# Kernel optimization log

Hardware: AMD Instinct MI355X
Metric: run time of the kernel (lower is better)

The kernel has to match this reference:

```python
import jax, jax.numpy as jnp
import numpy as np

B, T = 128, 512
D_IN, D_OUT, H = 12, 320, 64


def _conv1d(x, w, b, dilation):
    # x: [B,C,T], w: [O,I,K]  (torch Conv1d layout), 'same' padding for odd receptive field
    k = w.shape[-1]
    pad = ((k - 1) * dilation + 1) // 2
    y = jax.lax.conv_general_dilated(x, w, (1,), [(pad, pad)], rhs_dilation=(dilation,),
                                     dimension_numbers=('NCH', 'OIH', 'NCH'))
    return y + b[None, :, None]


def _gelu(x):
    return jax.nn.gelu(x, approximate=False)  # torch F.gelu default (erf)


def _encoder(x, c0_1_w, c0_1_b, c0_2_w, c0_2_b, c1_p_w, c1_p_b, c1_1_w, c1_1_b, c1_2_w, c1_2_b):
    # TS2Vec DilatedConvEncoder, channels=[64, 320], kernel=3. x: [B,T,64] -> [B,T,320]
    h = x.transpose(0, 2, 1)  # [B,64,T]
    # block 0: 64->64, dilation 1, identity residual
    res = h
    t = _conv1d(_gelu(h), c0_1_w, c0_1_b, 1)
    t = _conv1d(_gelu(t), c0_2_w, c0_2_b, 1)
    h = t + res
    # block 1: 64->320, dilation 2, final -> 1x1 projector residual
    res = _conv1d(h, c1_p_w, c1_p_b, 1)
    t = _conv1d(_gelu(h), c1_1_w, c1_1_b, 2)
    t = _conv1d(_gelu(t), c1_2_w, c1_2_b, 2)
    h = t + res
    return h.transpose(0, 2, 1)  # [B,T,320]


def _gru_cell(x, h, wih, whh, bih, bhh):
    # torch.nn.GRUCell math
    gi = x @ wih.T + bih  # [B,3H]
    gh = h @ whh.T + bhh
    i_r, i_z, i_n = jnp.split(gi, 3, axis=-1)
    h_r, h_z, h_n = jnp.split(gh, 3, axis=-1)
    r = jax.nn.sigmoid(i_r + h_r)
    z = jax.nn.sigmoid(i_z + h_z)
    n = jnp.tanh(i_n + r * h_n)
    return (1.0 - z) * n + z * h


def setup_inputs() -> dict:
    key = jax.random.key(0)
    ks = iter(jax.random.split(key, 40))
    f = lambda shape, s=0.05: (jax.random.normal(next(ks), shape, dtype=jnp.float32) * s)
    inp = {
        'x1': jax.random.normal(next(ks), (B, T, D_IN), dtype=jnp.float32),
        'x2': jax.random.normal(next(ks), (B, T, D_IN), dtype=jnp.float32),
        'X1': jax.random.normal(next(ks), (B, T, D_IN), dtype=jnp.float32),
        'X2': jax.random.normal(next(ks), (B, T, D_IN), dtype=jnp.float32),
        'X': jax.random.normal(next(ks), (B, T, D_IN), dtype=jnp.float32),
        'w_in': f((D_IN, H)), 'b_in': f((H,)),
        'c0_1_w': f((H, H, 3)), 'c0_1_b': f((H,)),
        'c0_2_w': f((H, H, 3)), 'c0_2_b': f((H,)),
        'c1_p_w': f((D_OUT, H, 1)), 'c1_p_b': f((D_OUT,)),
        'c1_1_w': f((D_OUT, H, 3)), 'c1_1_b': f((D_OUT,)),
        'c1_2_w': f((D_OUT, D_OUT, 3)), 'c1_2_b': f((D_OUT,)),
        'ih_dense_w': f((D_OUT, 4 * D_OUT)), 'ih_dense_b': f((4 * D_OUT,)),
        'ih_proj_w': f((4 * D_OUT, D_IN)), 'ih_proj_b': f((D_IN,)),
        'fc_w': f((D_IN, D_OUT)), 'fc_b': f((D_OUT,)),
        'gru_wih': f((3 * H, D_OUT)), 'gru_whh': f((3 * H, H)),
        'gru_bih': f((3 * H,)), 'gru_bhh': f((3 * H,)),
        'out_w': f((H, D_OUT)), 'out_b': f((D_OUT,)),
        'fcr_w': f((D_OUT, D_IN)), 'fcr_b': f((D_IN,)),
    }
    return inp


def reference(x1, x2, X1, X2, X, w_in, b_in, c0_1_w, c0_1_b, c0_2_w, c0_2_b,
              c1_p_w, c1_p_b, c1_1_w, c1_1_b, c1_2_w, c1_2_b,
              ih_dense_w, ih_dense_b, ih_proj_w, ih_proj_b,
              fc_w, fc_b, gru_wih, gru_whh, gru_bih, gru_bhh,
              out_w, out_b, fcr_w, fcr_b):
    conv_p = (c0_1_w, c0_1_b, c0_2_w, c0_2_b, c1_p_w, c1_p_b, c1_1_w, c1_1_b, c1_2_w, c1_2_b)
    m1 = (x1 != 0).astype(jnp.int32)
    m2 = (x2 != 0).astype(jnp.int32)
    enc = lambda a: _encoder(a @ w_in + b_in, *conv_p)  # dropout = identity (deterministic ref)
    x_whole1 = enc(X1)
    x_whole2 = enc(X2)

    def interp(a):
        r = enc(a)
        h = jax.nn.relu(r @ ih_dense_w + ih_dense_b)
        return h @ ih_proj_w + ih_proj_b  # [B,T,D_IN]

    x_interp1 = interp(x1)
    x_interp2 = interp(x2)
    mask1 = (~jnp.isnan(x_interp1).any(-1)).astype(jnp.float32)  # [B,T]

    y1 = x_interp1 @ fc_w + fc_b  # [B,T,320] (self.fc applied to every step at once)
    y2 = x_interp2 @ fc_w + fc_b
    h0 = jnp.zeros((x1.shape[0], gru_whh.shape[1]), x1.dtype)

    def step(carry, xs):
        h1, h2 = carry
        yt1, yt2, mt = xs
        h1 = _gru_cell(yt1, h1, gru_wih, gru_whh, gru_bih, gru_bhh)
        h2 = _gru_cell(yt2, h2, gru_wih, gru_whh, gru_bih, gru_bhh)
        o1 = h1 @ out_w + out_b
        o2 = h2 @ out_w + out_b
        keep = (mt == 1.0)[:, None]
        o1 = jnp.where(keep, yt1, o1)
        o2 = jnp.where(keep, yt1, o2)  # faithful: source uses mask1 / y_t1 for both
        return (h1, h2), (o1, o2)

    _, (o1, o2) = jax.lax.scan(step, (h0, h0),
                               (y1.transpose(1, 0, 2), y2.transpose(1, 0, 2), mask1.T))
    outputs2 = jax.lax.stop_gradient(o2.transpose(1, 0, 2)) @ fcr_w + fcr_b
    outputs1 = jax.lax.stop_gradient(o1.transpose(1, 0, 2)) @ fcr_w + fcr_b
    return (x_whole1, x_whole2, outputs1, outputs2, m1, m2, x1, x2)
```

## Files before the change

### kernel.cpp

```cpp
#include <hip/hip_runtime.h>
#include <hip/hip_bf16.h>
#include <math.h>


#define BB    128
#define TSEQ  512
#define NTILE 8
#define DIN   12
#define C0    64
#define C1    320
#define TT    64
#define PP    76
#define HALO  6
#define R64P  72
#define R320P 328

#define S1 ((size_t)BB * TSEQ * C1)
#define S2 ((size_t)BB * TSEQ * DIN)

typedef __attribute__((ext_vector_type(8))) __bf16 bf16x8;
typedef __attribute__((ext_vector_type(4))) float f32x4;
#define MFMA16(a, b, c) __builtin_amdgcn_mfma_f32_16x16x32_bf16(a, b, c, 0, 0, 0)

#define O01 0
#define O02 12288
#define O11 24576
#define O12 86016
#define OD  413696
#define OP  823296
#define NWS 843776
#define OGM 843776
#define OF2 844064

#define LA  0
#define LB  10944
#define LC  10944
#define LXI 55552
#define LGM 58624
#define LF2 59200
#define LSZ 59248
#define LRR 0
#define LZB 41984

__device__ __forceinline__ float bf2f(const __hip_bfloat16 v) { return __bfloat162float(v); }
__device__ __forceinline__ __hip_bfloat16 f2bf(float f)       { return __float2bfloat16(f); }
__device__ __forceinline__ float geluf(float x) {
    return 0.5f * x * (1.0f + erff(x * 0.7071067811865475f));
}
__device__ __forceinline__ bf16x8 ldb8(const void* p) { return *(const bf16x8*)p; }

extern "C" __global__ void __launch_bounds__(256) prep_w(
    const float* __restrict__ c01w, const float* __restrict__ c02w,
    const float* __restrict__ c11w, const float* __restrict__ c12w,
    const float* __restrict__ c1pw, const float* __restrict__ dw,
    const float* __restrict__ pw,
    const float* __restrict__ fcw,  const float* __restrict__ fcb,
    const float* __restrict__ fcrw, const float* __restrict__ fcrb,
    __hip_bfloat16* __restrict__ ws)
{
    for (size_t i = (size_t)blockIdx.x * 256 + threadIdx.x; i < NWS;
         i += (size_t)gridDim.x * 256) {
        float v;
        if (i < O02)      { int q = (int)i;        int n = q / 192, r = q % 192;
                            v = c01w[(n * 64 + (r & 63)) * 3 + (r >> 6)]; }
        else if (i < O11) { int q = (int)(i - O02); int n = q / 192, r = q % 192;
                            v = c02w[(n * 64 + (r & 63)) * 3 + (r >> 6)]; }
        else if (i < O12) { int q = (int)(i - O11); int n = q / 192, r = q % 192;
                            v = c11w[(n * 64 + (r & 63)) * 3 + (r >> 6)]; }
        else if (i < OD)  { int q = (int)(i - O12); int n = q >> 10, k = q & 1023;
                            v = (k < 960) ? c12w[(n * 320 + (k % 320)) * 3 + (k / 320)]
                                          : c1pw[n * 64 + (k - 960)]; }
        else if (i < OP)  { int q = (int)(i - OD);  int h = q / 320, c = q % 320;
                            v = dw[c * 1280 + h]; }
        else              { int q = (int)(i - OP);  int j = q / 1280, h = q % 1280;
                            v = (j < 12) ? pw[h * 12 + j] : 0.f; }
        ws[i] = f2bf(v);
    }
    if (blockIdx.x == 0) {
        float* gm = (float*)(ws + OGM);
        float* f2 = (float*)(ws + OF2);
        for (int o = threadIdx.x; o < 144; o += 256) {
            int j = o / 12, j2 = o - j * 12;
            float s = 0.f;
            for (int c = 0; c < C1; c++) s += fcw[j * C1 + c] * fcrw[c * 12 + j2];
            gm[o] = s;
        }
        if (threadIdx.x < 12) {
            float s = fcrb[threadIdx.x];
            for (int c = 0; c < C1; c++) s += fcb[c] * fcrw[c * 12 + threadIdx.x];
            f2[threadIdx.x] = s;
        }
    }
}

extern "C" __global__ void __launch_bounds__(256, 2) fused_main(
    const float* __restrict__ x1,  const float* __restrict__ X1,
    const float* __restrict__ X2,
    const float* __restrict__ w_in, const float* __restrict__ b_in,
    const float* __restrict__ c01b, const float* __restrict__ c02b,
    const float* __restrict__ c1pb, const float* __restrict__ c11b,
    const float* __restrict__ c12b,
    const float* __restrict__ db,   const float* __restrict__ pb,
    const __hip_bfloat16* __restrict__ ws,
    float* __restrict__ out)
{
    __shared__ __align__(16) unsigned char smem[LSZ];
    __hip_bfloat16* A  = (__hip_bfloat16*)(smem + LA);
    __hip_bfloat16* Bf = (__hip_bfloat16*)(smem + LB);
    __hip_bfloat16* C  = (__hip_bfloat16*)(smem + LC);
    float* XI = (float*)(smem + LXI);
    float* Gm = (float*)(smem + LGM);
    float* F2 = (float*)(smem + LF2);
    __hip_bfloat16* Rr = (__hip_bfloat16*)(smem + LRR);

    const int tid  = threadIdx.x;
    const int wv   = tid >> 6;
    const int lane = tid & 63;
    const int lm   = lane & 15;
    const int lq   = lane >> 4;
    const int bid  = blockIdx.x;
    const int pass = bid % 3;
    const int rem  = bid / 3;
    const int b    = rem >> 3;
    const int t0   = (rem & (NTILE - 1)) * TT;
    const float* xin = (pass == 0) ? X1 : (pass == 1) ? X2 : x1;

    const f32x4 Z4 = {0.f, 0.f, 0.f, 0.f};

    if (pass == 2) {
        const float* gmw = (const float*)(ws + OGM);
        const float* f2w = (const float*)(ws + OF2);
        for (int o = tid; o < 144; o += 256) Gm[o] = gmw[o];
        if (tid < 12) F2[tid] = f2w[tid];
        for (int o = tid; o < TT * 12; o += 256) XI[o] = pb[o % 12];
    }

    for (int o = tid; o < PP * C0; o += 256) {
        int p = o >> 6, c = o & 63;
        int t = t0 + p - HALO;
        float acc = 0.f;
        if (t >= 0 && t < TSEQ) {
            acc = b_in[c];
            const float4* xr4 = (const float4*)(xin + ((size_t)b * TSEQ + t) * DIN);
            float4 v0 = xr4[0], v1 = xr4[1], v2 = xr4[2];
            const float xv[12] = {v0.x, v0.y, v0.z, v0.w, v1.x, v1.y,
                                  v1.z, v1.w, v2.x, v2.y, v2.z, v2.w};
            #pragma unroll
            for (int i = 0; i < DIN; i++) acc += xv[i] * w_in[i * C0 + c];
        }
        A [p * R64P + c] = f2bf(acc);
        Bf[p * R64P + c] = f2bf(geluf(acc));
    }
    __syncthreads();

    {
        const int oc = wv * 16 + lm;
        f32x4 acc[5] = {Z4, Z4, Z4, Z4, Z4};
        #pragma unroll
        for (int ks = 0; ks < 6; ks++) {
            int tap = ks >> 1, ci = ((ks & 1) << 5) + (lq << 3);
            bf16x8 bf = ldb8(ws + O01 + oc * 192 + ks * 32 + (lq << 3));
            #pragma unroll
            for (int mt = 0; mt < 5; mt++) {
                int p = 1 + mt * 16 + lm + tap - 1; p = p > 75 ? 75 : p;
                acc[mt] = MFMA16(ldb8(Bf + p * R64P + ci), bf, acc[mt]);
            }
        }
        __syncthreads();
        float bias = c01b[oc];
        #pragma unroll
        for (int mt = 0; mt < 5; mt++)
            #pragma unroll
            for (int r = 0; r < 4; r++) {
                int m = mt * 16 + lq * 4 + r;
                if (m < 74) {
                    int p = 1 + m, t = t0 + p - HALO;
                    Bf[p * R64P + oc] =
                        f2bf((t >= 0 && t < TSEQ) ? geluf(acc[mt][r] + bias) : 0.f);
                }
            }
    }
    __syncthreads();

    {
        const int oc = wv * 16 + lm;
        f32x4 acc[5] = {Z4, Z4, Z4, Z4, Z4};
        #pragma unroll
        for (int ks = 0; ks < 6; ks++) {
            int tap = ks >> 1, ci = ((ks & 1) << 5) + (lq << 3);
            bf16x8 bf = ldb8(ws + O02 + oc * 192 + ks * 32 + (lq << 3));
            #pragma unroll
            for (int mt = 0; mt < 5; mt++) {
                int p = 2 + mt * 16 + lm + tap - 1; p = p > 75 ? 75 : p;
                acc[mt] = MFMA16(ldb8(Bf + p * R64P + ci), bf, acc[mt]);
            }
        }
        float resv[5][4];
        #pragma unroll
        for (int mt = 0; mt < 5; mt++)
            #pragma unroll
            for (int r = 0; r < 4; r++) {
                int m = mt * 16 + lq * 4 + r;
                resv[mt][r] = (m < 72) ? bf2f(A[(2 + m) * R64P + oc]) : 0.f;
            }
        __syncthreads();
        float bias = c02b[oc];
        #pragma unroll
        for (int mt = 0; mt < 5; mt++)
            #pragma unroll
            for (int r = 0; r < 4; r++) {
                int m = mt * 16 + lq * 4 + r;
                if (m < 72) {
                    int p = 2 + m, t = t0 + p - HALO;
                    bool v = (t >= 0 && t < TSEQ);
                    float hb = acc[mt][r] + bias + resv[mt][r];
                    A [p * R64P + oc] = f2bf(v ? hb : 0.f);
                    Bf[p * R64P + oc] = f2bf(v ? geluf(hb) : 0.f);
                }
            }
    }
    __syncthreads();

    {
        f32x4 acc[5][5];
        #pragma unroll
        for (int mt = 0; mt < 5; mt++)
            #pragma unroll
            for (int nt = 0; nt < 5; nt++) acc[mt][nt] = Z4;
        bf16x8 aa[5], ba[5], ab[5], bb[5];
        auto ld3 = [&](int ks, bf16x8 (&a)[5], bf16x8 (&bw)[5]) {
            int tap = ks >> 1, ci = ((ks & 1) << 5) + (lq << 3);
            #pragma unroll
            for (int mt = 0; mt < 5; mt++) {
                int p = 4 + mt * 16 + lm + 2 * (tap - 1); p = p > 75 ? 75 : p;
                a[mt] = ldb8(Bf + p * R64P + ci);
            }
            #pragma unroll
            for (int nt = 0; nt < 5; nt++)
                bw[nt] = ldb8(ws + O11 + (wv * 80 + nt * 16 + lm) * 192
                              + ks * 32 + (lq << 3));
        };
        ld3(0, aa, ba);
        #pragma unroll
        for (int ks = 0; ks < 6; ks += 2) {
            ld3(ks + 1, ab, bb);
            #pragma unroll
            for (int nt = 0; nt < 5; nt++)
                #pragma unroll
                for (int mt = 0; mt < 5; mt++)
                    acc[mt][nt] = MFMA16(aa[mt], ba[nt], acc[mt][nt]);
            if (ks + 2 < 6) ld3(ks + 2, aa, ba);
            #pragma unroll
            for (int nt = 0; nt < 5; nt++)
                #pragma unroll
                for (int mt = 0; mt < 5; mt++)
                    acc[mt][nt] = MFMA16(ab[mt], bb[nt], acc[mt][nt]);
        }
        __syncthreads();
        #pragma unroll
        for (int nt = 0; nt < 5; nt++) {
            int oc = wv * 80 + nt * 16 + lm;
            float bias = c11b[oc];
            #pragma unroll
            for (int mt = 0; mt < 5; mt++)
                #pragma unroll
                for (int r = 0; r < 4; r++) {
                    int m = mt * 16 + lq * 4 + r;
                    if (m < 68) {
                        int t = t0 + 4 + m - HALO;
                        C[m * R320P + oc] =
                            f2bf((t >= 0 && t < TSEQ) ? geluf(acc[mt][nt][r] + bias) : 0.f);
                    }
                }
        }
    }
    __syncthreads();

    {
        f32x4 acc[4][5];
        #pragma unroll
        for (int mt = 0; mt < 4; mt++)
            #pragma unroll
            for (int nt = 0; nt < 5; nt++) acc[mt][nt] = Z4;
        bf16x8 aa[4], ba[5], ab[4], bb[5];
        auto ld4 = [&](int ks, bf16x8 (&a)[4], bf16x8 (&bw)[5]) {
            if (ks < 30) {
                int tap = (ks >= 20) ? 2 : (ks >= 10 ? 1 : 0);
                int ci = (ks - tap * 10) * 32 + (lq << 3);
                #pragma unroll
                for (int mt = 0; mt < 4; mt++)
                    a[mt] = ldb8(C + (2 + mt * 16 + lm + 2 * (tap - 1)) * R320P + ci);
            } else {
                int ci = ((ks - 30) << 5) + (lq << 3);
                #pragma unroll
                for (int mt = 0; mt < 4; mt++)
                    a[mt] = ldb8(A + (6 + mt * 16 + lm) * R64P + ci);
            }
            #pragma unroll
            for (int nt = 0; nt < 5; nt++)
                bw[nt] = ldb8(ws + O12 + (wv * 80 + nt * 16 + lm) * 1024
                              + ks * 32 + (lq << 3));
        };
        ld4(0, aa, ba);
        for (int ks = 0; ks < 32; ks += 2) {
            ld4(ks + 1, ab, bb);
            #pragma unroll
            for (int nt = 0; nt < 5; nt++)
                #pragma unroll
                for (int mt = 0; mt < 4; mt++)
                    acc[mt][nt] = MFMA16(aa[mt], ba[nt], acc[mt][nt]);
            if (ks + 2 < 32) ld4(ks + 2, aa, ba);
            #pragma unroll
            for (int nt = 0; nt < 5; nt++)
                #pragma unroll
                for (int mt = 0; mt < 4; mt++)
                    acc[mt][nt] = MFMA16(ab[mt], bb[nt], acc[mt][nt]);
        }
        if (pass < 2) {
            #pragma unroll
            for (int nt = 0; nt < 5; nt++) {
                int oc = wv * 80 + nt * 16 + lm;
                float bias = c12b[oc] + c1pb[oc];
                const size_t obase = (pass == 1) ? S1 : (size_t)0;
                #pragma unroll
                for (int mt = 0; mt < 4; mt++)
                    #pragma unroll
                    for (int r = 0; r < 4; r++) {
                        int m = mt * 16 + lq * 4 + r;
                        out[obase + ((size_t)b * TSEQ + t0 + m) * C1 + oc] =
                            acc[mt][nt][r] + bias;
                    }
            }
        } else {
            __syncthreads();
            #pragma unroll
            for (int nt = 0; nt < 5; nt++) {
                int oc = wv * 80 + nt * 16 + lm;
                float bias = c12b[oc] + c1pb[oc];
                #pragma unroll
                for (int mt = 0; mt < 4; mt++)
                    #pragma unroll
                    for (int r = 0; r < 4; r++) {
                        int m = mt * 16 + lq * 4 + r;
                        Rr[m * R320P + oc] = f2bf(acc[mt][nt][r] + bias);
                    }
            }
            __syncthreads();
        }
    }

    if (pass == 2) {
        __hip_bfloat16* zb = (__hip_bfloat16*)(smem + LZB) + wv * (16 * R64P);
        f32x4 xacc[4] = {Z4, Z4, Z4, Z4};
        for (int cn = 0; cn < 5; cn++) {
            const int h0 = wv * 320 + cn * 64;
            f32x4 dacc[4][4];
            #pragma unroll
            for (int mt = 0; mt < 4; mt++)
                #pragma unroll
                for (int nt = 0; nt < 4; nt++) dacc[mt][nt] = Z4;
            bf16x8 aa[4], ba[4], ab[4], bb[4];
            auto ldd = [&](int ks, bf16x8 (&a)[4], bf16x8 (&bw)[4]) {
                int ci = ks * 32 + (lq << 3);
                #pragma unroll
                for (int mt = 0; mt < 4; mt++)
                    a[mt] = ldb8(Rr + (mt * 16 + lm) * R320P + ci);
                #pragma unroll
                for (int nt = 0; nt < 4; nt++)
                    bw[nt] = ldb8(ws + OD + (h0 + nt * 16 + lm) * 320 + ci);
            };
            ldd(0, aa, ba);
            #pragma unroll
            for (int ks = 0; ks < 10; ks += 2) {
                ldd(ks + 1, ab, bb);
                #pragma unroll
                for (int nt = 0; nt < 4; nt++)
                    #pragma unroll
                    for (int mt = 0; mt < 4; mt++)
                        dacc[mt][nt] = MFMA16(aa[mt], ba[nt], dacc[mt][nt]);
                if (ks + 2 < 10) ldd(ks + 2, aa, ba);
                #pragma unroll
                for (int nt = 0; nt < 4; nt++)
                    #pragma unroll
                    for (int mt = 0; mt < 4; mt++)
                        dacc[mt][nt] = MFMA16(ab[mt], bb[nt], dacc[mt][nt]);
            }
            #pragma unroll
            for (int mt = 0; mt < 4; mt++) {
                #pragma unroll
                for (int nt = 0; nt < 4; nt++) {
                    int h = h0 + nt * 16 + lm;
                    float dbv = db[h];
                    #pragma unroll
                    for (int r = 0; r < 4; r++)
                        zb[(lq * 4 + r) * R64P + nt * 16 + lm] =
                            f2bf(fmaxf(dacc[mt][nt][r] + dbv, 0.f));
                }
                #pragma unroll
                for (int k2 = 0; k2 < 2; k2++) {
                    int hl = k2 * 32 + (lq << 3);
                    bf16x8 bf = ldb8(ws + OP + lm * 1280 + h0 + hl);
                    xacc[mt] = MFMA16(ldb8(zb + lm * R64P + hl), bf, xacc[mt]);
                }
            }
        }
        if (lm < 12) {
            #pragma unroll
            for (int mt = 0; mt < 4; mt++)
                #pragma unroll
                for (int r = 0; r < 4; r++)
                    atomicAdd(&XI[(mt * 16 + lq * 4 + r) * 12 + lm], xacc[mt][r]);
        }
        __syncthreads();
        for (int o = tid; o < TT * 12; o += 256) {
            int p = o / 12, j2 = o - p * 12;
            float val = F2[j2];
            #pragma unroll
            for (int j = 0; j < 12; j++) val += XI[p * 12 + j] * Gm[j * 12 + j2];
            size_t idx = ((size_t)b * TSEQ + t0 + p) * DIN + j2;
            out[2 * S1 + idx]      = val;
            out[2 * S1 + S2 + idx] = val;
        }
    }
}

extern "C" __global__ void __launch_bounds__(256) tail_kernel(
    const float* __restrict__ x1, const float* __restrict__ x2,
    float* __restrict__ out)
{
    size_t i = (size_t)blockIdx.x * 256 + threadIdx.x;
    if (i >= S2) return;
    float a = x1[i], c = x2[i];
    const size_t base = 2 * S1 + 2 * S2;
    out[base + i]          = (a != 0.f) ? 1.f : 0.f;
    out[base + S2 + i]     = (c != 0.f) ? 1.f : 0.f;
    out[base + 2 * S2 + i] = a;
    out[base + 3 * S2 + i] = c;
}

extern "C" void kernel_launch(void* const* d_in, const int* in_sizes, int n_in,
                              void* d_out, int out_size, void* d_ws, size_t ws_size,
                              hipStream_t stream)
{
    (void)in_sizes; (void)n_in; (void)ws_size; (void)out_size;
    const float* x1   = (const float*)d_in[0];
    const float* x2   = (const float*)d_in[1];
    const float* X1   = (const float*)d_in[2];
    const float* X2   = (const float*)d_in[3];
    const float* w_in = (const float*)d_in[5];
    const float* b_in = (const float*)d_in[6];
    const float* c01w = (const float*)d_in[7];
    const float* c01b = (const float*)d_in[8];
    const float* c02w = (const float*)d_in[9];
    const float* c02b = (const float*)d_in[10];
    const float* c1pw = (const float*)d_in[11];
    const float* c1pb = (const float*)d_in[12];
    const float* c11w = (const float*)d_in[13];
    const float* c11b = (const float*)d_in[14];
    const float* c12w = (const float*)d_in[15];
    const float* c12b = (const float*)d_in[16];
    const float* dwp  = (const float*)d_in[17];
    const float* dbp  = (const float*)d_in[18];
    const float* pwp  = (const float*)d_in[19];
    const float* pbp  = (const float*)d_in[20];
    const float* fcw  = (const float*)d_in[21];
    const float* fcb  = (const float*)d_in[22];
    const float* fcrw = (const float*)d_in[29];
    const float* fcrb = (const float*)d_in[30];
    float* out = (float*)d_out;
    __hip_bfloat16* ws = (__hip_bfloat16*)d_ws;

    prep_w<<<824, 256, 0, stream>>>(c01w, c02w, c11w, c12w, c1pw, dwp, pwp,
                                    fcw, fcb, fcrw, fcrb, ws);

    fused_main<<<3 * BB * NTILE, 256, 0, stream>>>(
        x1, X1, X2, w_in, b_in, c01b, c02b, c1pb, c11b, c12b,
        dbp, pbp, ws, out);

    tail_kernel<<<(int)((S2 + 255) / 256), 256, 0, stream>>>(x1, x2, out);
}
```

Baseline: 826.0 us.

## Double workgroup to 512 threads and split M tiles across two wave groups

Each block now runs 8 waves instead of 4. Waves are split into four output-channel groups times two M-row groups, so each wave holds half as many accumulators across all conv, GEMM and decoder stages. Conv weights for the small layers are preloaded into registers, and the LDS layout grows to give each of the 8 waves its own zb scratch area. The aim is lower register pressure and more waves to hide latency. In exchange, each weight fragment is loaded from global memory by both M groups, and the 5-tile stages leave one group with uneven work.

```diff
diff --git a/kernel.cpp b/kernel.cpp
--- a/kernel.cpp
+++ b/kernel.cpp
@@ -35,10 +35,10 @@
 #define LA  0
 #define LB  10944
 #define LC  10944
-#define LXI 55552
-#define LGM 58624
-#define LF2 59200
-#define LSZ 59248
+#define LXI 60416
+#define LGM 63488
+#define LF2 64064
+#define LSZ 64112
 #define LRR 0
 #define LZB 41984
 
@@ -93,7 +93,7 @@
     }
 }
 
-extern "C" __global__ void __launch_bounds__(256, 2) fused_main(
+extern "C" __global__ void __launch_bounds__(512, 4) fused_main(
     const float* __restrict__ x1,  const float* __restrict__ X1,
     const float* __restrict__ X2,
     const float* __restrict__ w_in, const float* __restrict__ b_in,
@@ -115,6 +115,8 @@
 
     const int tid  = threadIdx.x;
     const int wv   = tid >> 6;
+    const int wg   = wv & 3;
+    const int mg   = wv >> 2;
     const int lane = tid & 63;
     const int lm   = lane & 15;
     const int lq   = lane >> 4;
@@ -130,12 +132,12 @@
     if (pass == 2) {
         const float* gmw = (const float*)(ws + OGM);
         const float* f2w = (const float*)(ws + OF2);
-        for (int o = tid; o < 144; o += 256) Gm[o] = gmw[o];
+        for (int o = tid; o < 144; o += 512) Gm[o] = gmw[o];
         if (tid < 12) F2[tid] = f2w[tid];
-        for (int o = tid; o < TT * 12; o += 256) XI[o] = pb[o % 12];
-    }
-
-    for (int o = tid; o < PP * C0; o += 256) {
+        for (int o = tid; o < TT * 12; o += 512) XI[o] = pb[o % 12];
+    }
+
+    for (int o = tid; o < PP * C0; o += 512) {
         int p = o >> 6, c = o & 63;
         int t = t0 + p - HALO;
         float acc = 0.f;
@@ -154,122 +156,87 @@
     __syncthreads();
 
     {
-        const int oc = wv * 16 + lm;
-        f32x4 acc[5] = {Z4, Z4, Z4, Z4, Z4};
+        const int oc = wg * 16 + lm;
+        bf16x8 bw[6];
+        #pragma unroll
+        for (int ks = 0; ks < 6; ks++)
+            bw[ks] = ldb8(ws + O01 + oc * 192 + ks * 32 + (lq << 3));
+        f32x4 acc[3] = {Z4, Z4, Z4};
         #pragma unroll
         for (int ks = 0; ks < 6; ks++) {
             int tap = ks >> 1, ci = ((ks & 1) << 5) + (lq << 3);
-            bf16x8 bf = ldb8(ws + O01 + oc * 192 + ks * 32 + (lq << 3));
-            #pragma unroll
-            for (int mt = 0; mt < 5; mt++) {
-                int p = 1 + mt * 16 + lm + tap - 1; p = p > 75 ? 75 : p;
-                acc[mt] = MFMA16(ldb8(Bf + p * R64P + ci), bf, acc[mt]);
+            #pragma unroll
+            for (int kk = 0; kk < 3; kk++) {
+                int mt = mg + 2 * kk;
+                if (mt < 5) {
+                    int p = 1 + mt * 16 + lm + tap - 1; p = p > 75 ? 75 : p;
+                    acc[kk] = MFMA16(ldb8(Bf + p * R64P + ci), bw[ks], acc[kk]);
+                }
             }
         }
         __syncthreads();
         float bias = c01b[oc];
         #pragma unroll
-        for (int mt = 0; mt < 5; mt++)
+        for (int kk = 0; kk < 3; kk++) {
+            int mt = mg + 2 * kk;
+            if (mt < 5)
+                #pragma unroll
+                for (int r = 0; r < 4; r++) {
+                    int m = mt * 16 + lq * 4 + r;
+                    if (m < 74) {
+                        int p = 1 + m, t = t0 + p - HALO;
+                        Bf[p * R64P + oc] =
+                            f2bf((t >= 0 && t < TSEQ) ? geluf(acc[kk][r] + bias) : 0.f);
+                    }
+                }
+        }
+    }
+    __syncthreads();
+
+    {
+        const int oc = wg * 16 + lm;
+        bf16x8 bw[6];
+        #pragma unroll
+        for (int ks = 0; ks < 6; ks++)
+            bw[ks] = ldb8(ws + O02 + oc * 192 + ks * 32 + (lq << 3));
+        f32x4 acc[3] = {Z4, Z4, Z4};
+        #pragma unroll
+        for (int ks = 0; ks < 6; ks++) {
+            int tap = ks >> 1, ci = ((ks & 1) << 5) + (lq << 3);
+            #pragma unroll
+            for (int kk = 0; kk < 3; kk++) {
+                int mt = mg + 2 * kk;
+                if (mt < 5) {
+                    int p = 2 + mt * 16 + lm + tap - 1; p = p > 75 ? 75 : p;
+                    acc[kk] = MFMA16(ldb8(Bf + p * R64P + ci), bw[ks], acc[kk]);
+                }
+            }
+        }
+        float resv[3][4];
+        #pragma unroll
+        for (int kk = 0; kk < 3; kk++) {
+            int mt = mg + 2 * kk;
             #pragma unroll
             for (int r = 0; r < 4; r++) {
                 int m = mt * 16 + lq * 4 + r;
-                if (m < 74) {
-                    int p = 1 + m, t = t0 + p - HALO;
-                    Bf[p * R64P + oc] =
-                        f2bf((t >= 0 && t < TSEQ) ? geluf(acc[mt][r] + bias) : 0.f);
-                }
-            }
-    }
-    __syncthreads();
-
-    {
-        const int oc = wv * 16 + lm;
-        f32x4 acc[5] = {Z4, Z4, Z4, Z4, Z4};
-        #pragma unroll
-        for (int ks = 0; ks < 6; ks++) {
-            int tap = ks >> 1, ci = ((ks & 1) << 5) + (lq << 3);
-            bf16x8 bf = ldb8(ws + O02 + oc * 192 + ks * 32 + (lq << 3));
-            #pragma unroll
-            for (int mt = 0; mt < 5; mt++) {
-                int p = 2 + mt * 16 + lm + tap - 1; p = p > 75 ? 75 : p;
-                acc[mt] = MFMA16(ldb8(Bf + p * R64P + ci), bf, acc[mt]);
-            }
-        }
-        float resv[5][4];
-        #pragma unroll
-        for (int mt = 0; mt < 5; mt++)
-            #pragma unroll
-            for (int r = 0; r < 4; r++) {
-                int m = mt * 16 + lq * 4 + r;
-                resv[mt][r] = (m < 72) ? bf2f(A[(2 + m) * R64P + oc]) : 0.f;
-            }
+                resv[kk][r] = (mt < 5 && m < 72) ? bf2f(A[(2 + m) * R64P + oc]) : 0.f;
+            }
+        }
         __syncthreads();
         float bias = c02b[oc];
         #pragma unroll
-        for (int mt = 0; mt < 5; mt++)
-            #pragma unroll
-            for (int r = 0; r < 4; r++) {
-                int m = mt * 16 + lq * 4 + r;
-                if (m < 72) {
-                    int p = 2 + m, t = t0 + p - HALO;
-                    bool v = (t >= 0 && t < TSEQ);
-                    float hb = acc[mt][r] + bias + resv[mt][r];
-                    A [p * R64P + oc] = f2bf(v ? hb : 0.f);
-                    Bf[p * R64P + oc] = f2bf(v ? geluf(hb) : 0.f);
-                }
-            }
-    }
-    __syncthreads();
-
-    {
-        f32x4 acc[5][5];
-        #pragma unroll
-        for (int mt = 0; mt < 5; mt++)
-            #pragma unroll
-            for (int nt = 0; nt < 5; nt++) acc[mt][nt] = Z4;
-        bf16x8 aa[5], ba[5], ab[5], bb[5];
-        auto ld3 = [&](int ks, bf16x8 (&a)[5], bf16x8 (&bw)[5]) {
-            int tap = ks >> 1, ci = ((ks & 1) << 5) + (lq << 3);
-            #pragma unroll
-            for (int mt = 0; mt < 5; mt++) {
-                int p = 4 + mt * 16 + lm + 2 * (tap - 1); p = p > 75 ? 75 : p;
-                a[mt] = ldb8(Bf + p * R64P + ci);
-            }
-            #pragma unroll
-            for (int nt = 0; nt < 5; nt++)
-                bw[nt] = ldb8(ws + O11 + (wv * 80 + nt * 16 + lm) * 192
-                              + ks * 32 + (lq << 3));
-        };
-        ld3(0, aa, ba);
-        #pragma unroll
-        for (int ks = 0; ks < 6; ks += 2) {
-            ld3(ks + 1, ab, bb);
-            #pragma unroll
-            for (int nt = 0; nt < 5; nt++)
-                #pragma unroll
-                for (int mt = 0; mt < 5; mt++)
-                    acc[mt][nt] = MFMA16(aa[mt], ba[nt], acc[mt][nt]);
-            if (ks + 2 < 6) ld3(ks + 2, aa, ba);
-            #pragma unroll
-            for (int nt = 0; nt < 5; nt++)
-                #pragma unroll
-                for (int mt = 0; mt < 5; mt++)
-                    acc[mt][nt] = MFMA16(ab[mt], bb[nt], acc[mt][nt]);
-        }
-        __syncthreads();
-        #pragma unroll
-        for (int nt = 0; nt < 5; nt++) {
-            int oc = wv * 80 + nt * 16 + lm;
-            float bias = c11b[oc];
-            #pragma unroll
-            for (int mt = 0; mt < 5; mt++)
+        for (int kk = 0; kk < 3; kk++) {
+            int mt = mg + 2 * kk;
+            if (mt < 5)
                 #pragma unroll
                 for (int r = 0; r < 4; r++) {
                     int m = mt * 16 + lq * 4 + r;
-                    if (m < 68) {
-                        int t = t0 + 4 + m - HALO;
-                        C[m * R320P + oc] =
-                            f2bf((t >= 0 && t < TSEQ) ? geluf(acc[mt][nt][r] + bias) : 0.f);
+                    if (m < 72) {
+                        int p = 2 + m, t = t0 + p - HALO;
+                        bool v = (t >= 0 && t < TSEQ);
+                        float hb = acc[kk][r] + bias + resv[kk][r];
+                        A [p * R64P + oc] = f2bf(v ? hb : 0.f);
+                        Bf[p * R64P + oc] = f2bf(v ? geluf(hb) : 0.f);
                     }
                 }
         }
@@ -277,28 +244,91 @@
     __syncthreads();
 
     {
-        f32x4 acc[4][5];
-        #pragma unroll
-        for (int mt = 0; mt < 4; mt++)
-            #pragma unroll
-            for (int nt = 0; nt < 5; nt++) acc[mt][nt] = Z4;
-        bf16x8 aa[4], ba[5], ab[4], bb[5];
-        auto ld4 = [&](int ks, bf16x8 (&a)[4], bf16x8 (&bw)[5]) {
+        f32x4 acc[3][5];
+        #pragma unroll
+        for (int kk = 0; kk < 3; kk++)
+            #pragma unroll
+            for (int nt = 0; nt < 5; nt++) acc[kk][nt] = Z4;
+        bf16x8 bcur[5], bnxt[5];
+        #pragma unroll
+        for (int nt = 0; nt < 5; nt++)
+            bcur[nt] = ldb8(ws + O11 + (wg * 80 + nt * 16 + lm) * 192 + (lq << 3));
+        #pragma unroll
+        for (int ks = 0; ks < 6; ks++) {
+            if (ks < 5)
+                #pragma unroll
+                for (int nt = 0; nt < 5; nt++)
+                    bnxt[nt] = ldb8(ws + O11 + (wg * 80 + nt * 16 + lm) * 192
+                                    + (ks + 1) * 32 + (lq << 3));
+            int tap = ks >> 1, ci = ((ks & 1) << 5) + (lq << 3);
+            bf16x8 a[3];
+            #pragma unroll
+            for (int kk = 0; kk < 3; kk++) {
+                int mt = mg + 2 * kk;
+                if (mt < 5) {
+                    int p = 4 + mt * 16 + lm + 2 * (tap - 1); p = p > 75 ? 75 : p;
+                    a[kk] = ldb8(Bf + p * R64P + ci);
+                }
+            }
+            #pragma unroll
+            for (int nt = 0; nt < 5; nt++)
+                #pragma unroll
+                for (int kk = 0; kk < 3; kk++)
+                    if (mg + 2 * kk < 5)
+                        acc[kk][nt] = MFMA16(a[kk], bcur[nt], acc[kk][nt]);
+            #pragma unroll
+            for (int nt = 0; nt < 5; nt++) bcur[nt] = bnxt[nt];
+        }
+        __syncthreads();
+        #pragma unroll
+        for (int nt = 0; nt < 5; nt++) {
+            int oc = wg * 80 + nt * 16 + lm;
+            float bias = c11b[oc];
+            #pragma unroll
+            for (int kk = 0; kk < 3; kk++) {
+                int mt = mg + 2 * kk;
+                if (mt < 5)
+                    #pragma unroll
+                    for (int r = 0; r < 4; r++) {
+                        int m = mt * 16 + lq * 4 + r;
+                        if (m < 68) {
+                            int t = t0 + 4 + m - HALO;
+                            C[m * R320P + oc] =
+                                f2bf((t >= 0 && t < TSEQ) ? geluf(acc[kk][nt][r] + bias) : 0.f);
+                        }
+                    }
+            }
+        }
+    }
+    __syncthreads();
+
+    {
+        f32x4 acc[2][5];
+        #pragma unroll
+        for (int kk = 0; kk < 2; kk++)
+            #pragma unroll
+            for (int nt = 0; nt < 5; nt++) acc[kk][nt] = Z4;
+        bf16x8 aa[2], ba[5], ab[2], bb[5];
+        auto ld4 = [&](int ks, bf16x8 (&a)[2], bf16x8 (&bw)[5]) {
             if (ks < 30) {
                 int tap = (ks >= 20) ? 2 : (ks >= 10 ? 1 : 0);
                 int ci = (ks - tap * 10) * 32 + (lq << 3);
                 #pragma unroll
-                for (int mt = 0; mt < 4; mt++)
-                    a[mt] = ldb8(C + (2 + mt * 16 + lm + 2 * (tap - 1)) * R320P + ci);
+                for (int kk = 0; kk < 2; kk++) {
+                    int mt = mg + 2 * kk;
+                    a[kk] = ldb8(C + (2 + mt * 16 + lm + 2 * (tap - 1)) * R320P + ci);
+                }
             } else {
                 int ci = ((ks - 30) << 5) + (lq << 3);
                 #pragma unroll
-                for (int mt = 0; mt < 4; mt++)
-                    a[mt] = ldb8(A + (6 + mt * 16 + lm) * R64P + ci);
+                for (int kk = 0; kk < 2; kk++) {
+                    int mt = mg + 2 * kk;
+                    a[kk] = ldb8(A + (6 + mt * 16 + lm) * R64P + ci);
+                }
             }
             #pragma unroll
             for (int nt = 0; nt < 5; nt++)
-                bw[nt] = ldb8(ws + O12 + (wv * 80 + nt * 16 + lm) * 1024
+                bw[nt] = ldb8(ws + O12 + (wg * 80 + nt * 16 + lm) * 1024
                               + ks * 32 + (lq << 3));
         };
         ld4(0, aa, ba);
@@ -307,43 +337,47 @@
             #pragma unroll
             for (int nt = 0; nt < 5; nt++)
                 #pragma unroll
-                for (int mt = 0; mt < 4; mt++)
-                    acc[mt][nt] = MFMA16(aa[mt], ba[nt], acc[mt][nt]);
+                for (int kk = 0; kk < 2; kk++)
+                    acc[kk][nt] = MFMA16(aa[kk], ba[nt], acc[kk][nt]);
             if (ks + 2 < 32) ld4(ks + 2, aa, ba);
             #pragma unroll
             for (int nt = 0; nt < 5; nt++)
                 #pragma unroll
-                for (int mt = 0; mt < 4; mt++)
-                    acc[mt][nt] = MFMA16(ab[mt], bb[nt], acc[mt][nt]);
+                for (int kk = 0; kk < 2; kk++)
+                    acc[kk][nt] = MFMA16(ab[kk], bb[nt], acc[kk][nt]);
         }
         if (pass < 2) {
             #pragma unroll
             for (int nt = 0; nt < 5; nt++) {
-                int oc = wv * 80 + nt * 16 + lm;
+                int oc = wg * 80 + nt * 16 + lm;
                 float bias = c12b[oc] + c1pb[oc];
                 const size_t obase = (pass == 1) ? S1 : (size_t)0;
                 #pragma unroll
-                for (int mt = 0; mt < 4; mt++)
+                for (int kk = 0; kk < 2; kk++) {
+                    int mt = mg + 2 * kk;
                     #pragma unroll
                     for (int r = 0; r < 4; r++) {
                         int m = mt * 16 + lq * 4 + r;
                         out[obase + ((size_t)b * TSEQ + t0 + m) * C1 + oc] =
-                            acc[mt][nt][r] + bias;
+                            acc[kk][nt][r] + bias;
                     }
+                }
             }
         } else {
             __syncthreads();
             #pragma unroll
             for (int nt = 0; nt < 5; nt++) {
-                int oc = wv * 80 + nt * 16 + lm;
+                int oc = wg * 80 + nt * 16 + lm;
                 float bias = c12b[oc] + c1pb[oc];
                 #pragma unroll
-                for (int mt = 0; mt < 4; mt++)
+                for (int kk = 0; kk < 2; kk++) {
+                    int mt = mg + 2 * kk;
                     #pragma unroll
                     for (int r = 0; r < 4; r++) {
                         int m = mt * 16 + lq * 4 + r;
-                        Rr[m * R320P + oc] = f2bf(acc[mt][nt][r] + bias);
+                        Rr[m * R320P + oc] = f2bf(acc[kk][nt][r] + bias);
                     }
+                }
             }
             __syncthreads();
         }
@@ -351,20 +385,20 @@
 
     if (pass == 2) {
         __hip_bfloat16* zb = (__hip_bfloat16*)(smem + LZB) + wv * (16 * R64P);
-        f32x4 xacc[4] = {Z4, Z4, Z4, Z4};
+        f32x4 xacc[2] = {Z4, Z4};
         for (int cn = 0; cn < 5; cn++) {
-            const int h0 = wv * 320 + cn * 64;
-            f32x4 dacc[4][4];
-            #pragma unroll
-            for (int mt = 0; mt < 4; mt++)
-                #pragma unroll
-                for (int nt = 0; nt < 4; nt++) dacc[mt][nt] = Z4;
-            bf16x8 aa[4], ba[4], ab[4], bb[4];
-            auto ldd = [&](int ks, bf16x8 (&a)[4], bf16x8 (&bw)[4]) {
+            const int h0 = wg * 320 + cn * 64;
+            f32x4 dacc[2][4];
+            #pragma unroll
+            for (int kk = 0; kk < 2; kk++)
+                #pragma unroll
+                for (int nt = 0; nt < 4; nt++) dacc[kk][nt] = Z4;
+            bf16x8 aa[2], ba[4], ab[2], bb[4];
+            auto ldd = [&](int ks, bf16x8 (&a)[2], bf16x8 (&bw)[4]) {
                 int ci = ks * 32 + (lq << 3);
                 #pragma unroll
-                for (int mt = 0; mt < 4; mt++)
-                    a[mt] = ldb8(Rr + (mt * 16 + lm) * R320P + ci);
+                for (int kk = 0; kk < 2; kk++)
+                    a[kk] = ldb8(Rr + ((mg + 2 * kk) * 16 + lm) * R320P + ci);
                 #pragma unroll
                 for (int nt = 0; nt < 4; nt++)
                     bw[nt] = ldb8(ws + OD + (h0 + nt * 16 + lm) * 320 + ci);
@@ -376,17 +410,17 @@
                 #pragma unroll
                 for (int nt = 0; nt < 4; nt++)
                     #pragma unroll
-                    for (int mt = 0; mt < 4; mt++)
-                        dacc[mt][nt] = MFMA16(aa[mt], ba[nt], dacc[mt][nt]);
+                    for (int kk = 0; kk < 2; kk++)
+                        dacc[kk][nt] = MFMA16(aa[kk], ba[nt], dacc[kk][nt]);
                 if (ks + 2 < 10) ldd(ks + 2, aa, ba);
                 #pragma unroll
                 for (int nt = 0; nt < 4; nt++)
                     #pragma unroll
-                    for (int mt = 0; mt < 4; mt++)
-                        dacc[mt][nt] = MFMA16(ab[mt], bb[nt], dacc[mt][nt]);
-            }
-            #pragma unroll
-            for (int mt = 0; mt < 4; mt++) {
+                    for (int kk = 0; kk < 2; kk++)
+                        dacc[kk][nt] = MFMA16(ab[kk], bb[nt], dacc[kk][nt]);
+            }
+            #pragma unroll
+            for (int kk = 0; kk < 2; kk++) {
                 #pragma unroll
                 for (int nt = 0; nt < 4; nt++) {
                     int h = h0 + nt * 16 + lm;
@@ -394,25 +428,27 @@
                     #pragma unroll
                     for (int r = 0; r < 4; r++)
                         zb[(lq * 4 + r) * R64P + nt * 16 + lm] =
-                            f2bf(fmaxf(dacc[mt][nt][r] + dbv, 0.f));
+                            f2bf(fmaxf(dacc[kk][nt][r] + dbv, 0.f));
                 }
                 #pragma unroll
                 for (int k2 = 0; k2 < 2; k2++) {
                     int hl = k2 * 32 + (lq << 3);
                     bf16x8 bf = ldb8(ws + OP + lm * 1280 + h0 + hl);
-                    xacc[mt] = MFMA16(ldb8(zb + lm * R64P + hl), bf, xacc[mt]);
+                    xacc[kk] = MFMA16(ldb8(zb + lm * R64P + hl), bf, xacc[kk]);
                 }
             }
         }
         if (lm < 12) {
             #pragma unroll
-            for (int mt = 0; mt < 4; mt++)
+            for (int kk = 0; kk < 2; kk++) {
+                int mt = mg + 2 * kk;
                 #pragma unroll
                 for (int r = 0; r < 4; r++)
-                    atomicAdd(&XI[(mt * 16 + lq * 4 + r) * 12 + lm], xacc[mt][r]);
+                    atomicAdd(&XI[(mt * 16 + lq * 4 + r) * 12 + lm], xacc[kk][r]);
+            }
         }
         __syncthreads();
-        for (int o = tid; o < TT * 12; o += 256) {
+        for (int o = tid; o < TT * 12; o += 512) {
             int p = o / 12, j2 = o - p * 12;
             float val = F2[j2];
             #pragma unroll
@@ -473,7 +509,7 @@
     prep_w<<<824, 256, 0, stream>>>(c01w, c02w, c11w, c12w, c1pw, dwp, pwp,
                                     fcw, fcb, fcrw, fcrb, ws);
 
-    fused_main<<<3 * BB * NTILE, 256, 0, stream>>>(
+    fused_main<<<3 * BB * NTILE, 512, 0, stream>>>(
         x1, X1, X2, w_in, b_in, c01b, c02b, c1pb, c11b, c12b,
         dbp, pbp, ws, out);
 
```

Measured after the change: 1.262 ms. 1.53x slower.

## Swizzle 320-wide LDS tiles, shrink LDS, and raise occupancy to three blocks

Applied to the files above, without the earlier changes.

Replaces the padded 328-element row layout of the C and Rr LDS buffers with an unpadded 640-byte row plus an XOR swizzle, which reduces LDS footprint and avoids bank conflicts. The smem layout is repacked, and the pass-2 constant loads move later so they reuse freed space. Launch bounds go from 2 to 3 blocks per CU. Register-level double buffering of LDS A operands is dropped in favour of loading A just before use, with weight-operand prefetch kept. The goal is more concurrent waves to hide latency, at the cost of tighter register budgets and possible spills.

```diff
diff --git a/kernel.cpp b/kernel.cpp
--- a/kernel.cpp
+++ b/kernel.cpp
@@ -13,7 +13,6 @@
 #define PP    76
 #define HALO  6
 #define R64P  72
-#define R320P 328
 
 #define S1 ((size_t)BB * TSEQ * C1)
 #define S2 ((size_t)BB * TSEQ * DIN)
@@ -33,14 +32,14 @@
 #define OF2 844064
 
 #define LA  0
-#define LB  10944
-#define LC  10944
-#define LXI 55552
-#define LGM 58624
-#define LF2 59200
-#define LSZ 59248
+#define LB  10656
+#define LC  10656
+#define LSZ 54176
 #define LRR 0
-#define LZB 41984
+#define LZB 40960
+#define LXI 50176
+#define LGM 53248
+#define LF2 53824
 
 __device__ __forceinline__ float bf2f(const __hip_bfloat16 v) { return __bfloat162float(v); }
 __device__ __forceinline__ __hip_bfloat16 f2bf(float f)       { return __float2bfloat16(f); }
@@ -48,6 +47,9 @@
     return 0.5f * x * (1.0f + erff(x * 0.7071067811865475f));
 }
 __device__ __forceinline__ bf16x8 ldb8(const void* p) { return *(const bf16x8*)p; }
+__device__ __forceinline__ void* swp(void* base, int row, int col) {
+    return (void*)((unsigned char*)base + (((row * 640 + col * 2)) ^ ((row & 7) << 4)));
+}
 
 extern "C" __global__ void __launch_bounds__(256) prep_w(
     const float* __restrict__ c01w, const float* __restrict__ c02w,
@@ -93,7 +95,7 @@
     }
 }
 
-extern "C" __global__ void __launch_bounds__(256, 2) fused_main(
+extern "C" __global__ void __launch_bounds__(256, 3) fused_main(
     const float* __restrict__ x1,  const float* __restrict__ X1,
     const float* __restrict__ X2,
     const float* __restrict__ w_in, const float* __restrict__ b_in,
@@ -107,11 +109,11 @@
     __shared__ __align__(16) unsigned char smem[LSZ];
     __hip_bfloat16* A  = (__hip_bfloat16*)(smem + LA);
     __hip_bfloat16* Bf = (__hip_bfloat16*)(smem + LB);
-    __hip_bfloat16* C  = (__hip_bfloat16*)(smem + LC);
+    unsigned char*  Cb = smem + LC;
+    unsigned char*  Rb = smem + LRR;
     float* XI = (float*)(smem + LXI);
     float* Gm = (float*)(smem + LGM);
     float* F2 = (float*)(smem + LF2);
-    __hip_bfloat16* Rr = (__hip_bfloat16*)(smem + LRR);
 
     const int tid  = threadIdx.x;
     const int wv   = tid >> 6;
@@ -127,14 +129,6 @@
 
     const f32x4 Z4 = {0.f, 0.f, 0.f, 0.f};
 
-    if (pass == 2) {
-        const float* gmw = (const float*)(ws + OGM);
-        const float* f2w = (const float*)(ws + OF2);
-        for (int o = tid; o < 144; o += 256) Gm[o] = gmw[o];
-        if (tid < 12) F2[tid] = f2w[tid];
-        for (int o = tid; o < TT * 12; o += 256) XI[o] = pb[o % 12];
-    }
-
     for (int o = tid; o < PP * C0; o += 256) {
         int p = o >> 6, c = o & 63;
         int t = t0 + p - HALO;
@@ -148,22 +142,25 @@
             #pragma unroll
             for (int i = 0; i < DIN; i++) acc += xv[i] * w_in[i * C0 + c];
         }
-        A [p * R64P + c] = f2bf(acc);
+        if (p < 74) A[p * R64P + c] = f2bf(acc);
         Bf[p * R64P + c] = f2bf(geluf(acc));
     }
     __syncthreads();
 
     {
         const int oc = wv * 16 + lm;
+        bf16x8 bw[6];
+        #pragma unroll
+        for (int ks = 0; ks < 6; ks++)
+            bw[ks] = ldb8(ws + O01 + oc * 192 + ks * 32 + (lq << 3));
         f32x4 acc[5] = {Z4, Z4, Z4, Z4, Z4};
         #pragma unroll
         for (int ks = 0; ks < 6; ks++) {
             int tap = ks >> 1, ci = ((ks & 1) << 5) + (lq << 3);
-            bf16x8 bf = ldb8(ws + O01 + oc * 192 + ks * 32 + (lq << 3));
             #pragma unroll
             for (int mt = 0; mt < 5; mt++) {
                 int p = 1 + mt * 16 + lm + tap - 1; p = p > 75 ? 75 : p;
-                acc[mt] = MFMA16(ldb8(Bf + p * R64P + ci), bf, acc[mt]);
+                acc[mt] = MFMA16(ldb8(Bf + p * R64P + ci), bw[ks], acc[mt]);
             }
         }
         __syncthreads();
@@ -184,15 +181,18 @@
 
     {
         const int oc = wv * 16 + lm;
+        bf16x8 bw[6];
+        #pragma unroll
+        for (int ks = 0; ks < 6; ks++)
+            bw[ks] = ldb8(ws + O02 + oc * 192 + ks * 32 + (lq << 3));
         f32x4 acc[5] = {Z4, Z4, Z4, Z4, Z4};
         #pragma unroll
         for (int ks = 0; ks < 6; ks++) {
             int tap = ks >> 1, ci = ((ks & 1) << 5) + (lq << 3);
-            bf16x8 bf = ldb8(ws + O02 + oc * 192 + ks * 32 + (lq << 3));
             #pragma unroll
             for (int mt = 0; mt < 5; mt++) {
                 int p = 2 + mt * 16 + lm + tap - 1; p = p > 75 ? 75 : p;
-                acc[mt] = MFMA16(ldb8(Bf + p * R64P + ci), bf, acc[mt]);
+                acc[mt] = MFMA16(ldb8(Bf + p * R64P + ci), bw[ks], acc[mt]);
             }
         }
         float resv[5][4];
@@ -227,34 +227,23 @@
         for (int mt = 0; mt < 5; mt++)
             #pragma unroll
             for (int nt = 0; nt < 5; nt++) acc[mt][nt] = Z4;
-        bf16x8 aa[5], ba[5], ab[5], bb[5];
-        auto ld3 = [&](int ks, bf16x8 (&a)[5], bf16x8 (&bw)[5]) {
+        #pragma unroll
+        for (int ks = 0; ks < 6; ks++) {
             int tap = ks >> 1, ci = ((ks & 1) << 5) + (lq << 3);
+            bf16x8 a[5];
             #pragma unroll
             for (int mt = 0; mt < 5; mt++) {
                 int p = 4 + mt * 16 + lm + 2 * (tap - 1); p = p > 75 ? 75 : p;
                 a[mt] = ldb8(Bf + p * R64P + ci);
             }
             #pragma unroll
-            for (int nt = 0; nt < 5; nt++)
-                bw[nt] = ldb8(ws + O11 + (wv * 80 + nt * 16 + lm) * 192
-                              + ks * 32 + (lq << 3));
-        };
-        ld3(0, aa, ba);
-        #pragma unroll
-        for (int ks = 0; ks < 6; ks += 2) {
-            ld3(ks + 1, ab, bb);
-            #pragma unroll
-            for (int nt = 0; nt < 5; nt++)
+            for (int nt = 0; nt < 5; nt++) {
+                bf16x8 bw = ldb8(ws + O11 + (wv * 80 + nt * 16 + lm) * 192
+                                 + ks * 32 + (lq << 3));
                 #pragma unroll
                 for (int mt = 0; mt < 5; mt++)
-                    acc[mt][nt] = MFMA16(aa[mt], ba[nt], acc[mt][nt]);
-            if (ks + 2 < 6) ld3(ks + 2, aa, ba);
-            #pragma unroll
-            for (int nt = 0; nt < 5; nt++)
-                #pragma unroll
-                for (int mt = 0; mt < 5; mt++)
-                    acc[mt][nt] = MFMA16(ab[mt], bb[nt], acc[mt][nt]);
+                    acc[mt][nt] = MFMA16(a[mt], bw, acc[mt][nt]);
+            }
         }
         __syncthreads();
         #pragma unroll
@@ -268,7 +257,7 @@
                     int m = mt * 16 + lq * 4 + r;
                     if (m < 68) {
                         int t = t0 + 4 + m - HALO;
-                        C[m * R320P + oc] =
+                        *(__hip_bfloat16*)swp(Cb, m, oc) =
                             f2bf((t >= 0 && t < TSEQ) ? geluf(acc[mt][nt][r] + bias) : 0.f);
                     }
                 }
@@ -279,42 +268,64 @@
     {
         f32x4 acc[4][5];
         #pragma unroll
-        for (int mt = 0; mt < 4; mt++)
-            #pragma unroll
-            for (int nt = 0; nt < 5; nt++) acc[mt][nt] = Z4;
-        bf16x8 aa[4], ba[5], ab[4], bb[5];
-        auto ld4 = [&](int ks, bf16x8 (&a)[4], bf16x8 (&bw)[5]) {
-            if (ks < 30) {
-                int tap = (ks >= 20) ? 2 : (ks >= 10 ? 1 : 0);
-                int ci = (ks - tap * 10) * 32 + (lq << 3);
-                #pragma unroll
-                for (int mt = 0; mt < 4; mt++)
-                    a[mt] = ldb8(C + (2 + mt * 16 + lm + 2 * (tap - 1)) * R320P + ci);
-            } else {
-                int ci = ((ks - 30) << 5) + (lq << 3);
-                #pragma unroll
-                for (int mt = 0; mt < 4; mt++)
-                    a[mt] = ldb8(A + (6 + mt * 16 + lm) * R64P + ci);
-            }
+        for (int kk = 0; kk < 4; kk++)
+            #pragma unroll
+            for (int nt = 0; nt < 5; nt++) acc[kk][nt] = Z4;
+        bf16x8 ba[5], bb[5];
+        #pragma unroll
+        for (int nt = 0; nt < 5; nt++)
+            ba[nt] = ldb8(ws + O12 + (wv * 80 + nt * 16 + lm) * 1024 + (lq << 3));
+        for (int ks = 0; ks < 32; ks += 2) {
             #pragma unroll
             for (int nt = 0; nt < 5; nt++)
-                bw[nt] = ldb8(ws + O12 + (wv * 80 + nt * 16 + lm) * 1024
-                              + ks * 32 + (lq << 3));
-        };
-        ld4(0, aa, ba);
-        for (int ks = 0; ks < 32; ks += 2) {
-            ld4(ks + 1, ab, bb);
-            #pragma unroll
-            for (int nt = 0; nt < 5; nt++)
-                #pragma unroll
-                for (int mt = 0; mt < 4; mt++)
-                    acc[mt][nt] = MFMA16(aa[mt], ba[nt], acc[mt][nt]);
-            if (ks + 2 < 32) ld4(ks + 2, aa, ba);
-            #pragma unroll
-            for (int nt = 0; nt < 5; nt++)
-                #pragma unroll
-                for (int mt = 0; mt < 4; mt++)
-                    acc[mt][nt] = MFMA16(ab[mt], bb[nt], acc[mt][nt]);
+                bb[nt] = ldb8(ws + O12 + (wv * 80 + nt * 16 + lm) * 1024
+                              + (ks + 1) * 32 + (lq << 3));
+            {
+                bf16x8 a[4];
+                if (ks < 30) {
+                    int tap = (ks >= 20) ? 2 : (ks >= 10 ? 1 : 0);
+                    int ci = (ks - tap * 10) * 32 + (lq << 3);
+                    #pragma unroll
+                    for (int mt = 0; mt < 4; mt++)
+                        a[mt] = ldb8(swp(Cb, 2 + mt * 16 + lm + 2 * (tap - 1), ci));
+                } else {
+                    int ci = ((ks - 30) << 5) + (lq << 3);
+                    #pragma unroll
+                    for (int mt = 0; mt < 4; mt++)
+                        a[mt] = ldb8(A + (6 + mt * 16 + lm) * R64P + ci);
+                }
+                #pragma unroll
+                for (int nt = 0; nt < 5; nt++)
+                    #pragma unroll
+                    for (int mt = 0; mt < 4; mt++)
+                        acc[mt][nt] = MFMA16(a[mt], ba[nt], acc[mt][nt]);
+            }
+            if (ks + 2 < 32)
+                #pragma unroll
+                for (int nt = 0; nt < 5; nt++)
+                    ba[nt] = ldb8(ws + O12 + (wv * 80 + nt * 16 + lm) * 1024
+                                  + (ks + 2) * 32 + (lq << 3));
+            {
+                int k1 = ks + 1;
+                bf16x8 a[4];
+                if (k1 < 30) {
+                    int tap = (k1 >= 20) ? 2 : (k1 >= 10 ? 1 : 0);
+                    int ci = (k1 - tap * 10) * 32 + (lq << 3);
+                    #pragma unroll
+                    for (int mt = 0; mt < 4; mt++)
+                        a[mt] = ldb8(swp(Cb, 2 + mt * 16 + lm + 2 * (tap - 1), ci));
+                } else {
+                    int ci = ((k1 - 30) << 5) + (lq << 3);
+                    #pragma unroll
+                    for (int mt = 0; mt < 4; mt++)
+                        a[mt] = ldb8(A + (6 + mt * 16 + lm) * R64P + ci);
+                }
+                #pragma unroll
+                for (int nt = 0; nt < 5; nt++)
+                    #pragma unroll
+                    for (int mt = 0; mt < 4; mt++)
+                        acc[mt][nt] = MFMA16(a[mt], bb[nt], acc[mt][nt]);
+            }
         }
         if (pass < 2) {
             #pragma unroll
@@ -342,9 +353,14 @@
                     #pragma unroll
                     for (int r = 0; r < 4; r++) {
                         int m = mt * 16 + lq * 4 + r;
-                        Rr[m * R320P + oc] = f2bf(acc[mt][nt][r] + bias);
+                        *(__hip_bfloat16*)swp(Rb, m, oc) = f2bf(acc[mt][nt][r] + bias);
                     }
             }
+            const float* gmw = (const float*)(ws + OGM);
+            const float* f2w = (const float*)(ws + OF2);
+            for (int o = tid; o < TT * 12; o += 256) XI[o] = pb[o % 12];
+            for (int o = tid; o < 144; o += 256) Gm[o] = gmw[o];
+            if (tid < 12) F2[tid] = f2w[tid];
             __syncthreads();
         }
     }
@@ -359,31 +375,42 @@
             for (int mt = 0; mt < 4; mt++)
                 #pragma unroll
                 for (int nt = 0; nt < 4; nt++) dacc[mt][nt] = Z4;
-            bf16x8 aa[4], ba[4], ab[4], bb[4];
-            auto ldd = [&](int ks, bf16x8 (&a)[4], bf16x8 (&bw)[4]) {
-                int ci = ks * 32 + (lq << 3);
-                #pragma unroll
-                for (int mt = 0; mt < 4; mt++)
-                    a[mt] = ldb8(Rr + (mt * 16 + lm) * R320P + ci);
+            bf16x8 ba[4], bb[4];
+            #pragma unroll
+            for (int nt = 0; nt < 4; nt++)
+                ba[nt] = ldb8(ws + OD + (h0 + nt * 16 + lm) * 320 + (lq << 3));
+            for (int ks = 0; ks < 10; ks += 2) {
                 #pragma unroll
                 for (int nt = 0; nt < 4; nt++)
-                    bw[nt] = ldb8(ws + OD + (h0 + nt * 16 + lm) * 320 + ci);
-            };
-            ldd(0, aa, ba);
-            #pragma unroll
-            for (int ks = 0; ks < 10; ks += 2) {
-                ldd(ks + 1, ab, bb);
-                #pragma unroll
-                for (int nt = 0; nt < 4; nt++)
-                    #pragma unroll
-                    for (int mt = 0; mt < 4; mt++)
-                        dacc[mt][nt] = MFMA16(aa[mt], ba[nt], dacc[mt][nt]);
-                if (ks + 2 < 10) ldd(ks + 2, aa, ba);
-                #pragma unroll
-                for (int nt = 0; nt < 4; nt++)
-                    #pragma unroll
-                    for (int mt = 0; mt < 4; mt++)
-                        dacc[mt][nt] = MFMA16(ab[mt], bb[nt], dacc[mt][nt]);
+                    bb[nt] = ldb8(ws + OD + (h0 + nt * 16 + lm) * 320
+                                  + (ks + 1) * 32 + (lq << 3));
+                {
+                    bf16x8 a[4];
+                    #pragma unroll
+                    for (int mt = 0; mt < 4; mt++)
+                        a[mt] = ldb8(swp(Rb, mt * 16 + lm, ks * 32 + (lq << 3)));
+                    #pragma unroll
+                    for (int nt = 0; nt < 4; nt++)
+                        #pragma unroll
+                        for (int mt = 0; mt < 4; mt++)
+                            dacc[mt][nt] = MFMA16(a[mt], ba[nt], dacc[mt][nt]);
+                }
+                if (ks + 2 < 10)
+                    #pragma unroll
+                    for (int nt = 0; nt < 4; nt++)
+                        ba[nt] = ldb8(ws + OD + (h0 + nt * 16 + lm) * 320
+                                      + (ks + 2) * 32 + (lq << 3));
+                {
+                    bf16x8 a[4];
+                    #pragma unroll
+                    for (int mt = 0; mt < 4; mt++)
+                        a[mt] = ldb8(swp(Rb, mt * 16 + lm, (ks + 1) * 32 + (lq << 3)));
+                    #pragma unroll
+                    for (int nt = 0; nt < 4; nt++)
+                        #pragma unroll
+                        for (int mt = 0; mt < 4; mt++)
+                            dacc[mt][nt] = MFMA16(a[mt], bb[nt], dacc[mt][nt]);
+                }
             }
             #pragma unroll
             for (int mt = 0; mt < 4; mt++) {
```

After: 933.9 us. 1.13x slower.
